# Optimization experiments

Hardware: AMD Instinct MI355X
Metric: run time of the kernel (lower is better)

## Reference

```python
import jax, jax.numpy as jnp
import numpy as np

B, S, T = 128, 1024, 512
VOCAB, E, HE, HD, ATT = 1000, 128, 64, 66, 32


def setup_inputs() -> dict:
    key = jax.random.key(0)
    ks = jax.random.split(key, 14)
    p = lambda k, shape: (jax.random.normal(k, shape, dtype=jnp.float32) * 0.05)
    return {
        'x': jax.random.randint(ks[0], (B, S), 0, VOCAB, dtype=jnp.int32),
        'c': jax.random.normal(ks[1], (B, T), dtype=jnp.float32),
        'emb': p(ks[2], (VOCAB, E)),
        'enc_Wih': p(ks[3], (4 * HE, E)),
        'enc_Whh': p(ks[4], (4 * HE, HE)),
        'enc_b': p(ks[5], (4 * HE,)),
        'att_fc_W': p(ks[6], (HE, E)),
        'att_fc_b': p(ks[7], (HE,)),
        'att_w_W': p(ks[8], (ATT, HE)),
        'att_w_b': p(ks[9], (ATT,)),
        'dec_Wih': p(ks[10], (4 * HD, ATT)),
        'dec_Whh': p(ks[11], (4 * HD, HD)),
        'dec_b': p(ks[12], (4 * HD,)),
        'fin_W': p(ks[13], (E, HD)),
        'fin_b': jnp.zeros((E,), dtype=jnp.float32),
    }


def _lstm_seq(xs, W_ih, W_hh, b, H):
    # xs: [B, S, in]; PyTorch gate order i, f, g, o
    bsz = xs.shape[0]
    gx = jnp.einsum('bsi,gi->bsg', xs, W_ih) + b  # [B,S,4H]

    def step(carry, g_t):
        h, c = carry
        g = g_t + h @ W_hh.T
        i, f, gg, o = jnp.split(g, 4, axis=-1)
        c = jax.nn.sigmoid(f) * c + jax.nn.sigmoid(i) * jnp.tanh(gg)
        h = jax.nn.sigmoid(o) * jnp.tanh(c)
        return (h, c), h

    h0 = jnp.zeros((bsz, H), xs.dtype)
    (_, _), hs = jax.lax.scan(step, (h0, h0), jnp.swapaxes(gx, 0, 1))
    return jnp.swapaxes(hs, 0, 1)  # [B,S,H]


def reference(x, c, emb, enc_Wih, enc_Whh, enc_b, att_fc_W, att_fc_b,
              att_w_W, att_w_b, dec_Wih, dec_Whh, dec_b, fin_W, fin_b):
    # encoder: embed + LSTM, returns full sequence of hidden states [B,S,64]
    enc = _lstm_seq(emb[x], enc_Wih, enc_Whh, enc_b, HE)
    bsz, steps = x.shape[0], c.shape[1]
    # initial decoder input: embedding of token 0, broadcast over batch
    x0 = jnp.broadcast_to(emb[0], (bsz, E))
    h0 = jnp.zeros((bsz, HD), enc.dtype)

    def step(carry, _):
        xemb, h, cc = carry
        # attend(a=xemb, A=enc)
        a = xemb @ att_fc_W.T + att_fc_b                     # [B,64]
        A = a[:, None, :] * enc                              # [B,S,64]
        alpha = jax.nn.softmax(
            jnp.tanh(jnp.einsum('bse,ae->bsa', A, att_w_W) + att_w_b),
            axis=-1)                                         # [B,S,32]
        beta = alpha.sum(axis=1)                             # [B,32]
        # decoder LSTM cell (one timestep)
        g = beta @ dec_Wih.T + h @ dec_Whh.T + dec_b
        i, f, gg, o = jnp.split(g, 4, axis=-1)
        cc = jax.nn.sigmoid(f) * cc + jax.nn.sigmoid(i) * jnp.tanh(gg)
        h = jax.nn.sigmoid(o) * jnp.tanh(cc)
        xemb = h @ fin_W.T + fin_b                           # feed back via final_fc
        return (xemb, h, cc), h

    _, hs = jax.lax.scan(step, (x0, h0, h0), None, length=steps)
    return jnp.swapaxes(hs, 0, 1)  # [B,T,66]
```

## Files before the change

### kernel.cpp

```cpp
#include <hip/hip_runtime.h>
#include <hip/hip_bf16.h>

#define kB 128
#define kS 1024
#define kT 512
#define kV 1000
#define kE 128
#define kHE 64
#define kHD 66
#define kATT 32
#define kGE 256
#define kGD 264

typedef __attribute__((ext_vector_type(4))) float f32x4;
typedef __attribute__((ext_vector_type(8))) short bf16x8;
typedef __attribute__((ext_vector_type(8))) unsigned short u16x8;

__device__ __forceinline__ unsigned short f2bf(float f) {
  unsigned int u = __builtin_bit_cast(unsigned int, f);
  u += 0x7FFFu + ((u >> 16) & 1u);
  return (unsigned short)(u >> 16);
}
__device__ __forceinline__ float rcp_(float x) { return __builtin_amdgcn_rcpf(x); }
__device__ __forceinline__ float fsig(float x)  { return rcp_(1.0f + __expf(-x)); }
__device__ __forceinline__ float ftanh(float x) { return 1.0f - 2.0f * rcp_(1.0f + __expf(2.0f * x)); }
__device__ __forceinline__ float fexp2(float z) {
#if __has_builtin(__builtin_amdgcn_exp2f)
  return __builtin_amdgcn_exp2f(z);
#else
  return __expf(z * 0.6931471805599453f);
#endif
}
__device__ __forceinline__ const unsigned short* launder_us(const unsigned short* p) {
  asm volatile("" : "+s"(p));
  return p;
}
__device__ __forceinline__ float dpp_red16(float v) {
  int x = __builtin_bit_cast(int, v);
  v += __builtin_bit_cast(float, __builtin_amdgcn_update_dpp(0, x, 0xB1, 0xf, 0xf, true));
  x = __builtin_bit_cast(int, v);
  v += __builtin_bit_cast(float, __builtin_amdgcn_update_dpp(0, x, 0x4E, 0xf, 0xf, true));
  x = __builtin_bit_cast(int, v);
  v += __builtin_bit_cast(float, __builtin_amdgcn_update_dpp(0, x, 0x124, 0xf, 0xf, true));
  x = __builtin_bit_cast(int, v);
  v += __builtin_bit_cast(float, __builtin_amdgcn_update_dpp(0, x, 0x128, 0xf, 0xf, true));
  return v;
}
#define DPPB(v, ctrl) __builtin_bit_cast(float, __builtin_amdgcn_update_dpp(0, __builtin_bit_cast(int, (v)), (ctrl), 0xf, 0xf, true))

__global__ __launch_bounds__(256) void prep_kernel(
    const float* __restrict__ emb, const float* __restrict__ enc_Wih,
    const float* __restrict__ enc_b, const float* __restrict__ enc_Whh,
    const float* __restrict__ att_fc_W, const float* __restrict__ att_fc_b,
    const float* __restrict__ att_w_W,
    const float* __restrict__ fin_W, const float* __restrict__ fin_b,
    const float* __restrict__ dec_Wih, const float* __restrict__ dec_Whh,
    const float* __restrict__ dec_b,
    float* __restrict__ embW, unsigned short* __restrict__ decF,
    unsigned short* __restrict__ encF, unsigned short* __restrict__ afF,
    float* __restrict__ wregF, float* __restrict__ dbias,
    float* __restrict__ wh64, float* __restrict__ wh65,
    float* __restrict__ abias, float* __restrict__ ainit) {
  int bid = blockIdx.x, tid = threadIdx.x;
  if (bid < kV) {
    float acc = enc_b[tid];
    const float* er = emb + bid * kE;
    const float* wr = enc_Wih + tid * kE;
    for (int e = 0; e < kE; ++e) acc += er[e] * wr[e];
    embW[bid * kGE + tid] = acc;
  } else if (bid == kV) {
    for (int i = tid; i < 17 * 3 * 64 * 8; i += 256) {
      int jj = i & 7, lane = (i >> 3) & 63, ts = i >> 9;
      int tile = ts / 3, ks = ts - tile * 3;
      int jp = tile * 16 + (lane & 15);
      int cell = jp >> 2, gate = jp & 3;
      int k = ks * 32 + ((lane >> 4) << 3) + jj;
      float v = 0.f;
      if (cell < kHD) {
        int j = gate * kHD + cell;
        if (k < 32) v = dec_Wih[j * kATT + k];
        else v = dec_Whh[j * kHD + (k - 32)];
      }
      decF[i] = f2bf(v);
    }
  } else if (bid == kV + 1) {
    for (int i = tid; i < 16 * 2 * 64 * 8; i += 256) {
      int jj = i & 7, lane = (i >> 3) & 63, ts = i >> 9;
      int tile = ts >> 1, ks = ts & 1;
      int j = tile * 16 + (lane & 15);
      int k = ks * 32 + ((lane >> 4) << 3) + jj;
      encF[i] = f2bf(enc_Whh[j * kHE + k]);
    }
  } else if (bid == kV + 2) {
    for (int i = tid; i < 4 * 3 * 64 * 8; i += 256) {
      int jj = i & 7, lane = (i >> 3) & 63, ts = i >> 9;
      int tile = ts / 3, ks = ts - tile * 3;
      int aidx = tile * 16 + (lane & 15);
      int m = ks * 32 + ((lane >> 4) << 3) + jj;
      float v = 0.f;
      if (m < kHD)
        for (int e = 0; e < kE; ++e) v += att_fc_W[aidx * kE + e] * fin_W[e * kHD + m];
      afF[i] = f2bf(v);
    }
  } else if (bid == kV + 3) {
    for (int i = tid; i < 8 * 64 * 4; i += 256) {
      int c = i & 3, lane = (i >> 2) & 63, jq = i >> 8;
      int half = jq & 1, kc = (jq >> 1) & 1, mt = jq >> 2;
      wregF[i] = att_w_W[(mt * 16 + (lane & 15)) * kHE + kc * 32 + ((lane >> 4) << 3) + half * 4 + c];
    }
  } else if (bid == kV + 4) {
    for (int jp = tid; jp < kGD; jp += 256) {
      int cell = jp >> 2, gate = jp & 3;
      int j = gate * kHD + cell;
      float s = 0.f;
      for (int m = 0; m < kATT; ++m) s += dec_Wih[j * kATT + m];
      dbias[jp] = dec_b[j] + 32.0f * s;
      wh64[jp] = dec_Whh[j * kHD + 64];
      wh65[jp] = dec_Whh[j * kHD + 65];
    }
  } else {
    if (tid < kHE) {
      float acc = att_fc_b[tid];
      for (int e = 0; e < kE; ++e) acc += att_fc_W[tid * kE + e] * fin_b[e];
      abias[tid] = acc;
    } else if (tid < 2 * kHE) {
      int a = tid - kHE;
      float acc = att_fc_b[a];
      for (int e = 0; e < kE; ++e) acc += emb[e] * att_fc_W[a * kE + e];
      ainit[a] = acc;
    }
  }
}

__global__ __launch_bounds__(256)
__attribute__((amdgpu_waves_per_eu(1, 1)))
void enc_kernel(
    const int* __restrict__ x, const float* __restrict__ embW,
    const unsigned short* __restrict__ encF, float* __restrict__ out) {
  __shared__ struct __align__(16) {
    unsigned short xe[64];
    float gbuf[kGE];
    int toks[kS];
  } sm;
  const int b = blockIdx.x, t = threadIdx.x, lane = t & 63, wv = t >> 6;

  for (int i = t; i < kS; i += 256) sm.toks[i] = x[b * kS + i];
  if (t < 64) sm.xe[t] = 0;

  u16x8 eQ[4][2];
  #pragma unroll
  for (int q = 0; q < 4; ++q)
    #pragma unroll
    for (int ks = 0; ks < 2; ++ks)
      eQ[q][ks] = *(const u16x8*)&encF[(((wv * 4 + q) * 2 + ks) * 64 + lane) * 8];
  __syncthreads();

  float gx0 = 0, gx1 = 0, gx2 = 0, gx3 = 0;
  if (lane < 16) {
    int tok = sm.toks[0];
    gx0 = embW[tok * kGE + wv * 64 + 0 + lane];
    gx1 = embW[tok * kGE + wv * 64 + 16 + lane];
    gx2 = embW[tok * kGE + wv * 64 + 32 + lane];
    gx3 = embW[tok * kGE + wv * 64 + 48 + lane];
  }
  float cE = 0.0f;
  unsigned short* eg = (unsigned short*)(out + (size_t)b * (kT * kHD));

  for (int s = 0; s < kS; ++s) {
    union { u16x8 u; bf16x8 v; } xa0, xa1;
    xa0.u = *(const u16x8*)&sm.xe[(lane >> 4) << 3];
    xa1.u = *(const u16x8*)&sm.xe[32 + ((lane >> 4) << 3)];
    float gn0 = 0, gn1 = 0, gn2 = 0, gn3 = 0;
    int tokn = sm.toks[(s + 1 < kS) ? (s + 1) : s];
    if (lane < 16) {
      gn0 = embW[tokn * kGE + wv * 64 + 0 + lane];
      gn1 = embW[tokn * kGE + wv * 64 + 16 + lane];
      gn2 = embW[tokn * kGE + wv * 64 + 32 + lane];
      gn3 = embW[tokn * kGE + wv * 64 + 48 + lane];
    }
    f32x4 z = {0.f, 0.f, 0.f, 0.f};
    f32x4 a0 = __builtin_amdgcn_mfma_f32_16x16x32_bf16(xa0.v, eQ[0][0], z, 0, 0, 0);
    a0 = __builtin_amdgcn_mfma_f32_16x16x32_bf16(xa1.v, eQ[0][1], a0, 0, 0, 0);
    f32x4 a1 = __builtin_amdgcn_mfma_f32_16x16x32_bf16(xa0.v, eQ[1][0], z, 0, 0, 0);
    a1 = __builtin_amdgcn_mfma_f32_16x16x32_bf16(xa1.v, eQ[1][1], a1, 0, 0, 0);
    f32x4 a2 = __builtin_amdgcn_mfma_f32_16x16x32_bf16(xa0.v, eQ[2][0], z, 0, 0, 0);
    a2 = __builtin_amdgcn_mfma_f32_16x16x32_bf16(xa1.v, eQ[2][1], a2, 0, 0, 0);
    f32x4 a3 = __builtin_amdgcn_mfma_f32_16x16x32_bf16(xa0.v, eQ[3][0], z, 0, 0, 0);
    a3 = __builtin_amdgcn_mfma_f32_16x16x32_bf16(xa1.v, eQ[3][1], a3, 0, 0, 0);
    if (lane < 16) {
      sm.gbuf[wv * 64 + 0 + lane]  = a0[0] + gx0;
      sm.gbuf[wv * 64 + 16 + lane] = a1[0] + gx1;
      sm.gbuf[wv * 64 + 32 + lane] = a2[0] + gx2;
      sm.gbuf[wv * 64 + 48 + lane] = a3[0] + gx3;
    }
    __syncthreads();
    if (t < 64) {
      float gi = sm.gbuf[t], gf = sm.gbuf[64 + t], gg = sm.gbuf[128 + t], go = sm.gbuf[192 + t];
      cE = fsig(gf) * cE + fsig(gi) * ftanh(gg);
      float h = fsig(go) * ftanh(cE);
      unsigned short hb = f2bf(h);
      sm.xe[t] = hb;
      eg[s * 64 + ((((t >> 3) ^ (s & 7)) << 3) | (t & 7))] = hb;
    }
    __syncthreads();
    gx0 = gn0; gx1 = gn1; gx2 = gn2; gx3 = gn3;
  }
}

struct __align__(16) DSm {
  unsigned short enc[kS * kHE];
  float wregL[8 * 64 * 4];
  unsigned short afL[4 * 3 * 64 * 8];
  float dbL[kGD];
  float wh64L[kGD];
  float wh65L[kGD];
  float absL[64];
  float aa[64];
  float beta[32];
  unsigned short xv[2][160];
  float hh2[2][2];
};

union U8 { u16x8 u; bf16x8 v; };

__global__ __launch_bounds__(512, 2)
void dec_kernel(
    const float* __restrict__ att_w_b,
    const unsigned short* __restrict__ decF, const unsigned short* __restrict__ afF,
    const float* __restrict__ wregF_ws, const float* __restrict__ dbias_ws,
    const float* __restrict__ wh64_ws, const float* __restrict__ wh65_ws,
    const float* __restrict__ abias_ws, const float* __restrict__ ainit_ws,
    float* __restrict__ out) {
  __shared__ DSm sm;
  const int b = blockIdx.x, t = threadIdx.x, lane = t & 63, wv = t >> 6;
  const int lr = lane & 15, g = lane >> 4;

  {
    const u16x8* src = (const u16x8*)(out + (size_t)b * (kT * kHD));
    u16x8* dst = (u16x8*)sm.enc;
    #pragma unroll
    for (int i = 0; i < 16; ++i) dst[t + i * 512] = src[t + i * 512];
  }
  ((f32x4*)sm.wregL)[t] = ((const f32x4*)wregF_ws)[t];
  for (int i = t; i < 768; i += 512) ((u16x8*)sm.afL)[i] = ((const u16x8*)afF)[i];
  for (int i = t; i < kGD; i += 512) {
    sm.dbL[i] = dbias_ws[i];
    sm.wh64L[i] = wh64_ws[i];
    sm.wh65L[i] = wh65_ws[i];
  }
  if (t < 64) { sm.absL[t] = abias_ws[t]; sm.aa[t] = ainit_ws[t]; }
  if (t < 32) sm.beta[t] = 0.f;
  for (int i = t; i < 320; i += 512) ((unsigned short*)sm.xv)[i] = 0;
  if (t < 4) ((float*)sm.hh2)[t] = 0.f;

  f32x4 wb0, wb1;
  #pragma unroll
  for (int r = 0; r < 4; ++r) {
    wb0[r] = att_w_b[g * 4 + r];
    wb1[r] = att_w_b[16 + g * 4 + r];
  }
  float cDa = 0.0f, cDb = 0.0f, cDc = 0.0f;
  __syncthreads();

  const int sbase = wv * 128;
  const int tileA = wv, tileB = wv + 8;
  const bool has3 = (wv == 7);

  for (int step = 0; step < kT; ++step) {
    const int cb = step & 1, nb = cb ^ 1;
    U8 qa[3], qb[3], qc[3];
    {
      const f32x4* aap = (const f32x4*)sm.aa;
      const f32x4* wrl = (const f32x4*)sm.wregL;
      bf16x8 af[2][2];
      #pragma unroll
      for (int kc = 0; kc < 2; ++kc) {
        f32x4 a0v = aap[kc * 8 + g * 2];
        f32x4 a1v = aap[kc * 8 + g * 2 + 1];
        #pragma unroll
        for (int mt = 0; mt < 2; ++mt) {
          f32x4 w0 = wrl[((mt * 2 + kc) * 2 + 0) * 64 + lane];
          f32x4 w1 = wrl[((mt * 2 + kc) * 2 + 1) * 64 + lane];
          union { bf16x8 v; __hip_bfloat162 h2[4]; } tmp;
          tmp.h2[0] = __float22bfloat162_rn(make_float2(w0.x * a0v.x, w0.y * a0v.y));
          tmp.h2[1] = __float22bfloat162_rn(make_float2(w0.z * a0v.z, w0.w * a0v.w));
          tmp.h2[2] = __float22bfloat162_rn(make_float2(w1.x * a1v.x, w1.y * a1v.y));
          tmp.h2[3] = __float22bfloat162_rn(make_float2(w1.z * a1v.z, w1.w * a1v.w));
          af[mt][kc] = tmp.v;
        }
      }
      float betaAcc[2][4] = {};
      float amax = 0.0f;
      #pragma unroll
      for (int nt = 0; nt < 8; ++nt) {
        int s = sbase + nt * 16 + lr;
        int sw = s & 7;
        U8 e0, e1;
        e0.u = *(const u16x8*)&sm.enc[s * kHE + ((g ^ sw) << 3)];
        e1.u = *(const u16x8*)&sm.enc[s * kHE + (((4 + g) ^ sw) << 3)];
        f32x4 acc0 = __builtin_amdgcn_mfma_f32_16x16x32_bf16(af[0][0], e0.v, wb0, 0, 0, 0);
        acc0 = __builtin_amdgcn_mfma_f32_16x16x32_bf16(af[0][1], e1.v, acc0, 0, 0, 0);
        f32x4 acc1 = __builtin_amdgcn_mfma_f32_16x16x32_bf16(af[1][0], e0.v, wb1, 0, 0, 0);
        acc1 = __builtin_amdgcn_mfma_f32_16x16x32_bf16(af[1][1], e1.v, acc1, 0, 0, 0);
        float u0[4], u1[4], dsum = 0.f;
        #pragma unroll
        for (int r = 0; r < 4; ++r) {
          float x0 = acc0[r], x1 = acc1[r];
          amax = fmaxf(amax, fmaxf(__builtin_fabsf(x0), __builtin_fabsf(x1)));
          u0[r] = fexp2(x0 * __builtin_fmaf(x0 * x0, -0.48089835f, 1.44269504f));
          u1[r] = fexp2(x1 * __builtin_fmaf(x1 * x1, -0.48089835f, 1.44269504f));
          dsum += u0[r] + u1[r];
        }
        dsum += __shfl_xor(dsum, 16);
        dsum += __shfl_xor(dsum, 32);
        float invd = rcp_(dsum);
        #pragma unroll
        for (int r = 0; r < 4; ++r) {
          betaAcc[0][r] += u0[r] * invd;
          betaAcc[1][r] += u1[r] * invd;
        }
      }
      if (__builtin_expect(__any(amax > 0.35f), 0)) {
        #pragma unroll
        for (int mt = 0; mt < 2; ++mt)
          #pragma unroll
          for (int r = 0; r < 4; ++r) betaAcc[mt][r] = 0.f;
        for (int nt = 0; nt < 8; ++nt) {
          int s = sbase + nt * 16 + lr;
          int sw = s & 7;
          U8 e0, e1;
          e0.u = *(const u16x8*)&sm.enc[s * kHE + ((g ^ sw) << 3)];
          e1.u = *(const u16x8*)&sm.enc[s * kHE + (((4 + g) ^ sw) << 3)];
          f32x4 acc0 = __builtin_amdgcn_mfma_f32_16x16x32_bf16(af[0][0], e0.v, wb0, 0, 0, 0);
          acc0 = __builtin_amdgcn_mfma_f32_16x16x32_bf16(af[0][1], e1.v, acc0, 0, 0, 0);
          f32x4 acc1 = __builtin_amdgcn_mfma_f32_16x16x32_bf16(af[1][0], e0.v, wb1, 0, 0, 0);
          acc1 = __builtin_amdgcn_mfma_f32_16x16x32_bf16(af[1][1], e1.v, acc1, 0, 0, 0);
          float u0[4], u1[4], dsum = 0.f;
          for (int r = 0; r < 4; ++r) {
            u0[r] = __expf(tanhf(acc0[r]));
            u1[r] = __expf(tanhf(acc1[r]));
            dsum += u0[r] + u1[r];
          }
          dsum += __shfl_xor(dsum, 16);
          dsum += __shfl_xor(dsum, 32);
          float invd = rcp_(dsum);
          for (int r = 0; r < 4; ++r) {
            betaAcc[0][r] += u0[r] * invd;
            betaAcc[1][r] += u1[r] * invd;
          }
        }
      }
      {
        const unsigned short* dFp = launder_us(decF);
        #pragma unroll
        for (int ks = 0; ks < 3; ++ks) {
          qa[ks].u = *(const u16x8*)&dFp[((tileA * 3 + ks) * 64 + lane) * 8];
          qb[ks].u = *(const u16x8*)&dFp[((tileB * 3 + ks) * 64 + lane) * 8];
        }
        if (has3) {
          #pragma unroll
          for (int ks = 0; ks < 3; ++ks)
            qc[ks].u = *(const u16x8*)&dFp[((16 * 3 + ks) * 64 + lane) * 8];
        }
      }
      #pragma unroll
      for (int mt = 0; mt < 2; ++mt)
        #pragma unroll
        for (int r = 0; r < 4; ++r) {
          float v = dpp_red16(betaAcc[mt][r]);
          if (lr == 0) atomicAdd(&sm.beta[mt * 16 + g * 4 + r], v);
        }
    }
    __syncthreads();
    {
      const f32x4* pb = (const f32x4*)sm.beta;
      f32x4 b0 = pb[g * 2], b1 = pb[g * 2 + 1];
      union { bf16x8 v; __hip_bfloat162 h2[4]; } bfr;
      bfr.h2[0] = __float22bfloat162_rn(make_float2(b0.x - 32.f, b0.y - 32.f));
      bfr.h2[1] = __float22bfloat162_rn(make_float2(b0.z - 32.f, b0.w - 32.f));
      bfr.h2[2] = __float22bfloat162_rn(make_float2(b1.x - 32.f, b1.y - 32.f));
      bfr.h2[3] = __float22bfloat162_rn(make_float2(b1.z - 32.f, b1.w - 32.f));
      U8 xg1, xg2;
      xg1.u = *(const u16x8*)&sm.xv[cb][32 + (g << 3)];
      xg2.u = *(const u16x8*)&sm.xv[cb][64 + (g << 3)];
      float hh0 = sm.hh2[cb][0], hh1 = sm.hh2[cb][1];
      float* op = out + ((size_t)b * kT + step) * kHD;
      const int gate = lane & 3;
      const float kk = (gate == 2) ? 2.0f : 1.0f;
      f32x4 z = {0.f, 0.f, 0.f, 0.f};
      {
        f32x4 ga = __builtin_amdgcn_mfma_f32_16x16x32_bf16(bfr.v, qa[0].v, z, 0, 0, 0);
        ga = __builtin_amdgcn_mfma_f32_16x16x32_bf16(xg1.v, qa[1].v, ga, 0, 0, 0);
        ga = __builtin_amdgcn_mfma_f32_16x16x32_bf16(xg2.v, qa[2].v, ga, 0, 0, 0);
        int jp = tileA * 16 + lr;
        float xg = ga[0] + sm.dbL[jp] + sm.wh64L[jp] * hh0 + sm.wh65L[jp] * hh1;
        float y = fsig(kk * xg);
        float v = (gate == 2) ? (2.0f * y - 1.0f) : y;
        float q0 = DPPB(v, 0x00), q1 = DPPB(v, 0x55), q2 = DPPB(v, 0xAA), q3 = DPPB(v, 0xFF);
        float cn = q1 * cDa + q0 * q2;
        cDa = cn;
        float h = q3 * ftanh(cn);
        if (gate == 0 && lane < 16) {
          int cell = jp >> 2;
          sm.xv[nb][32 + cell] = f2bf(h);
          op[cell] = h;
        }
      }
      {
        f32x4 gb = __builtin_amdgcn_mfma_f32_16x16x32_bf16(bfr.v, qb[0].v, z, 0, 0, 0);
        gb = __builtin_amdgcn_mfma_f32_16x16x32_bf16(xg1.v, qb[1].v, gb, 0, 0, 0);
        gb = __builtin_amdgcn_mfma_f32_16x16x32_bf16(xg2.v, qb[2].v, gb, 0, 0, 0);
        int jp = tileB * 16 + lr;
        float xg = gb[0] + sm.dbL[jp] + sm.wh64L[jp] * hh0 + sm.wh65L[jp] * hh1;
        float y = fsig(kk * xg);
        float v = (gate == 2) ? (2.0f * y - 1.0f) : y;
        float q0 = DPPB(v, 0x00), q1 = DPPB(v, 0x55), q2 = DPPB(v, 0xAA), q3 = DPPB(v, 0xFF);
        float cn = q1 * cDb + q0 * q2;
        cDb = cn;
        float h = q3 * ftanh(cn);
        if (gate == 0 && lane < 16) {
          int cell = jp >> 2;
          sm.xv[nb][32 + cell] = f2bf(h);
          op[cell] = h;
        }
      }
      if (has3) {
        f32x4 gc = __builtin_amdgcn_mfma_f32_16x16x32_bf16(bfr.v, qc[0].v, z, 0, 0, 0);
        gc = __builtin_amdgcn_mfma_f32_16x16x32_bf16(xg1.v, qc[1].v, gc, 0, 0, 0);
        gc = __builtin_amdgcn_mfma_f32_16x16x32_bf16(xg2.v, qc[2].v, gc, 0, 0, 0);
        int jp = 256 + (lane & 7);
        float xg = gc[0] + sm.dbL[jp] + sm.wh64L[jp] * hh0 + sm.wh65L[jp] * hh1;
        float y = fsig(kk * xg);
        float v = (gate == 2) ? (2.0f * y - 1.0f) : y;
        float q0 = DPPB(v, 0x00), q1 = DPPB(v, 0x55), q2 = DPPB(v, 0xAA), q3 = DPPB(v, 0xFF);
        float cn = q1 * cDc + q0 * q2;
        cDc = cn;
        float h = q3 * ftanh(cn);
        if (gate == 0 && lane < 8) {
          int cell = 64 + (lane >> 2);
          sm.xv[nb][32 + cell] = f2bf(h);
          sm.hh2[nb][lane >> 2] = h;
          op[cell] = h;
        }
      }
    }
    __syncthreads();
    if (wv == 0) {
      U8 y0, y1, y2;
      y0.u = *(const u16x8*)&sm.xv[nb][32 + (g << 3)];
      y1.u = *(const u16x8*)&sm.xv[nb][64 + (g << 3)];
      y2.u = *(const u16x8*)&sm.xv[nb][96 + (g << 3)];
      f32x4 z = {0.f, 0.f, 0.f, 0.f};
      #pragma unroll
      for (int tt = 0; tt < 4; ++tt) {
        U8 f0, f1, f2;
        f0.u = *(const u16x8*)&sm.afL[((tt * 3 + 0) * 64 + lane) * 8];
        f1.u = *(const u16x8*)&sm.afL[((tt * 3 + 1) * 64 + lane) * 8];
        f2.u = *(const u16x8*)&sm.afL[((tt * 3 + 2) * 64 + lane) * 8];
        f32x4 acc = __builtin_amdgcn_mfma_f32_16x16x32_bf16(y0.v, f0.v, z, 0, 0, 0);
        acc = __builtin_amdgcn_mfma_f32_16x16x32_bf16(y1.v, f1.v, acc, 0, 0, 0);
        acc = __builtin_amdgcn_mfma_f32_16x16x32_bf16(y2.v, f2.v, acc, 0, 0, 0);
        if (lane < 16) sm.aa[tt * 16 + lane] = acc[0] + sm.absL[tt * 16 + lane];
      }
      if (lane < 32) sm.beta[lane] = 0.f;
    }
    __syncthreads();
  }
}

extern "C" void kernel_launch(void* const* d_in, const int* in_sizes, int n_in,
                              void* d_out, int out_size, void* d_ws, size_t ws_size,
                              hipStream_t stream) {
  const int*   x        = (const int*)d_in[0];
  const float* emb      = (const float*)d_in[2];
  const float* enc_Wih  = (const float*)d_in[3];
  const float* enc_Whh  = (const float*)d_in[4];
  const float* enc_b    = (const float*)d_in[5];
  const float* att_fc_W = (const float*)d_in[6];
  const float* att_fc_b = (const float*)d_in[7];
  const float* att_w_W  = (const float*)d_in[8];
  const float* att_w_b  = (const float*)d_in[9];
  const float* dec_Wih  = (const float*)d_in[10];
  const float* dec_Whh  = (const float*)d_in[11];
  const float* dec_b    = (const float*)d_in[12];
  const float* fin_W    = (const float*)d_in[13];
  const float* fin_b    = (const float*)d_in[14];
  float* out = (float*)d_out;

  float* embW = (float*)d_ws;
  unsigned short* decF = (unsigned short*)(embW + kV * kGE);
  unsigned short* encF = decF + 17 * 3 * 64 * 8;
  unsigned short* afF  = encF + 16 * 2 * 64 * 8;
  float* wregF = (float*)(afF + 4 * 3 * 64 * 8);
  float* dbias = wregF + 8 * 64 * 4;
  float* wh64  = dbias + kGD;
  float* wh65  = wh64 + kGD;
  float* abias = wh65 + kGD;
  float* ainit = abias + kHE;

  prep_kernel<<<dim3(kV + 6), dim3(256), 0, stream>>>(
      emb, enc_Wih, enc_b, enc_Whh, att_fc_W, att_fc_b, att_w_W, fin_W, fin_b,
      dec_Wih, dec_Whh, dec_b, embW, decF, encF, afF, wregF, dbias, wh64, wh65,
      abias, ainit);
  enc_kernel<<<dim3(kB), dim3(256), 0, stream>>>(x, embW, encF, out);
  dec_kernel<<<dim3(kB), dim3(512), 0, stream>>>(
      att_w_b, decF, afF, wregF, dbias, wh64, wh65, abias, ainit, out);
}
```

Measured before the change: 2.823 ms.

## Transpose attention MFMA, split final_fc across four waves with register weights

Swaps the MFMA operands in the attention scoring so each lane holds one attention channel across sequence rows. The softmax denominator then becomes a 16-lane DPP reduction per row, and beta accumulates as two scalars per lane, reduced with two shuffles before the atomics. The final_fc/att_fc projection that fed the next step was done serially by wave 0 over four tiles. It is now split across waves 0-3, each keeping its weight fragment in registers instead of LDS, and wave 4 clears beta. This shortens the serial tail of each decoder step at the cost of more rcp/DPP work per tile and extra registers.

```diff
diff --git a/kernel.cpp b/kernel.cpp
--- a/kernel.cpp
+++ b/kernel.cpp
@@ -210,7 +210,6 @@
 struct __align__(16) DSm {
   unsigned short enc[kS * kHE];
   float wregL[8 * 64 * 4];
-  unsigned short afL[4 * 3 * 64 * 8];
   float dbL[kGD];
   float wh64L[kGD];
   float wh65L[kGD];
@@ -242,7 +241,6 @@
     for (int i = 0; i < 16; ++i) dst[t + i * 512] = src[t + i * 512];
   }
   ((f32x4*)sm.wregL)[t] = ((const f32x4*)wregF_ws)[t];
-  for (int i = t; i < 768; i += 512) ((u16x8*)sm.afL)[i] = ((const u16x8*)afF)[i];
   for (int i = t; i < kGD; i += 512) {
     sm.dbL[i] = dbias_ws[i];
     sm.wh64L[i] = wh64_ws[i];
@@ -253,11 +251,13 @@
   for (int i = t; i < 320; i += 512) ((unsigned short*)sm.xv)[i] = 0;
   if (t < 4) ((float*)sm.hh2)[t] = 0.f;
 
-  f32x4 wb0, wb1;
-  #pragma unroll
-  for (int r = 0; r < 4; ++r) {
-    wb0[r] = att_w_b[g * 4 + r];
-    wb1[r] = att_w_b[16 + g * 4 + r];
+  const float bw0 = att_w_b[lr];
+  const float bw1 = att_w_b[16 + lr];
+  U8 aQ[3];
+  if (wv < 4) {
+    #pragma unroll
+    for (int ks = 0; ks < 3; ++ks)
+      aQ[ks].u = *(const u16x8*)&afF[((wv * 3 + ks) * 64 + lane) * 8];
   }
   float cDa = 0.0f, cDb = 0.0f, cDc = 0.0f;
   __syncthreads();
@@ -289,7 +289,9 @@
           af[mt][kc] = tmp.v;
         }
       }
-      float betaAcc[2][4] = {};
+      f32x4 wc0 = {bw0, bw0, bw0, bw0};
+      f32x4 wc1 = {bw1, bw1, bw1, bw1};
+      float betaAcc[2] = {0.f, 0.f};
       float amax = 0.0f;
       #pragma unroll
       for (int nt = 0; nt < 8; ++nt) {
@@ -298,55 +300,46 @@
         U8 e0, e1;
         e0.u = *(const u16x8*)&sm.enc[s * kHE + ((g ^ sw) << 3)];
         e1.u = *(const u16x8*)&sm.enc[s * kHE + (((4 + g) ^ sw) << 3)];
-        f32x4 acc0 = __builtin_amdgcn_mfma_f32_16x16x32_bf16(af[0][0], e0.v, wb0, 0, 0, 0);
-        acc0 = __builtin_amdgcn_mfma_f32_16x16x32_bf16(af[0][1], e1.v, acc0, 0, 0, 0);
-        f32x4 acc1 = __builtin_amdgcn_mfma_f32_16x16x32_bf16(af[1][0], e0.v, wb1, 0, 0, 0);
-        acc1 = __builtin_amdgcn_mfma_f32_16x16x32_bf16(af[1][1], e1.v, acc1, 0, 0, 0);
-        float u0[4], u1[4], dsum = 0.f;
+        f32x4 acc0 = __builtin_amdgcn_mfma_f32_16x16x32_bf16(e0.v, af[0][0], wc0, 0, 0, 0);
+        acc0 = __builtin_amdgcn_mfma_f32_16x16x32_bf16(e1.v, af[0][1], acc0, 0, 0, 0);
+        f32x4 acc1 = __builtin_amdgcn_mfma_f32_16x16x32_bf16(e0.v, af[1][0], wc1, 0, 0, 0);
+        acc1 = __builtin_amdgcn_mfma_f32_16x16x32_bf16(e1.v, af[1][1], acc1, 0, 0, 0);
+        float u0[4], u1[4];
         #pragma unroll
         for (int r = 0; r < 4; ++r) {
           float x0 = acc0[r], x1 = acc1[r];
           amax = fmaxf(amax, fmaxf(__builtin_fabsf(x0), __builtin_fabsf(x1)));
           u0[r] = fexp2(x0 * __builtin_fmaf(x0 * x0, -0.48089835f, 1.44269504f));
           u1[r] = fexp2(x1 * __builtin_fmaf(x1 * x1, -0.48089835f, 1.44269504f));
-          dsum += u0[r] + u1[r];
-        }
-        dsum += __shfl_xor(dsum, 16);
-        dsum += __shfl_xor(dsum, 32);
-        float invd = rcp_(dsum);
+        }
         #pragma unroll
         for (int r = 0; r < 4; ++r) {
-          betaAcc[0][r] += u0[r] * invd;
-          betaAcc[1][r] += u1[r] * invd;
+          float invd = rcp_(dpp_red16(u0[r] + u1[r]));
+          betaAcc[0] += u0[r] * invd;
+          betaAcc[1] += u1[r] * invd;
         }
       }
       if (__builtin_expect(__any(amax > 0.35f), 0)) {
-        #pragma unroll
-        for (int mt = 0; mt < 2; ++mt)
-          #pragma unroll
-          for (int r = 0; r < 4; ++r) betaAcc[mt][r] = 0.f;
+        betaAcc[0] = 0.f; betaAcc[1] = 0.f;
         for (int nt = 0; nt < 8; ++nt) {
           int s = sbase + nt * 16 + lr;
           int sw = s & 7;
           U8 e0, e1;
           e0.u = *(const u16x8*)&sm.enc[s * kHE + ((g ^ sw) << 3)];
           e1.u = *(const u16x8*)&sm.enc[s * kHE + (((4 + g) ^ sw) << 3)];
-          f32x4 acc0 = __builtin_amdgcn_mfma_f32_16x16x32_bf16(af[0][0], e0.v, wb0, 0, 0, 0);
-          acc0 = __builtin_amdgcn_mfma_f32_16x16x32_bf16(af[0][1], e1.v, acc0, 0, 0, 0);
-          f32x4 acc1 = __builtin_amdgcn_mfma_f32_16x16x32_bf16(af[1][0], e0.v, wb1, 0, 0, 0);
-          acc1 = __builtin_amdgcn_mfma_f32_16x16x32_bf16(af[1][1], e1.v, acc1, 0, 0, 0);
-          float u0[4], u1[4], dsum = 0.f;
+          f32x4 acc0 = __builtin_amdgcn_mfma_f32_16x16x32_bf16(e0.v, af[0][0], wc0, 0, 0, 0);
+          acc0 = __builtin_amdgcn_mfma_f32_16x16x32_bf16(e1.v, af[0][1], acc0, 0, 0, 0);
+          f32x4 acc1 = __builtin_amdgcn_mfma_f32_16x16x32_bf16(e0.v, af[1][0], wc1, 0, 0, 0);
+          acc1 = __builtin_amdgcn_mfma_f32_16x16x32_bf16(e1.v, af[1][1], acc1, 0, 0, 0);
+          float u0[4], u1[4];
           for (int r = 0; r < 4; ++r) {
             u0[r] = __expf(tanhf(acc0[r]));
             u1[r] = __expf(tanhf(acc1[r]));
-            dsum += u0[r] + u1[r];
           }
-          dsum += __shfl_xor(dsum, 16);
-          dsum += __shfl_xor(dsum, 32);
-          float invd = rcp_(dsum);
           for (int r = 0; r < 4; ++r) {
-            betaAcc[0][r] += u0[r] * invd;
-            betaAcc[1][r] += u1[r] * invd;
+            float invd = rcp_(dpp_red16(u0[r] + u1[r]));
+            betaAcc[0] += u0[r] * invd;
+            betaAcc[1] += u1[r] * invd;
           }
         }
       }
@@ -364,12 +357,12 @@
         }
       }
       #pragma unroll
-      for (int mt = 0; mt < 2; ++mt)
-        #pragma unroll
-        for (int r = 0; r < 4; ++r) {
-          float v = dpp_red16(betaAcc[mt][r]);
-          if (lr == 0) atomicAdd(&sm.beta[mt * 16 + g * 4 + r], v);
-        }
+      for (int mt = 0; mt < 2; ++mt) {
+        float v = betaAcc[mt];
+        v += __shfl_xor(v, 16);
+        v += __shfl_xor(v, 32);
+        if (lane < 16) atomicAdd(&sm.beta[mt * 16 + lane], v);
+      }
     }
     __syncthreads();
     {
@@ -445,23 +438,17 @@
       }
     }
     __syncthreads();
-    if (wv == 0) {
+    if (wv < 4) {
       U8 y0, y1, y2;
       y0.u = *(const u16x8*)&sm.xv[nb][32 + (g << 3)];
       y1.u = *(const u16x8*)&sm.xv[nb][64 + (g << 3)];
       y2.u = *(const u16x8*)&sm.xv[nb][96 + (g << 3)];
       f32x4 z = {0.f, 0.f, 0.f, 0.f};
-      #pragma unroll
-      for (int tt = 0; tt < 4; ++tt) {
-        U8 f0, f1, f2;
-        f0.u = *(const u16x8*)&sm.afL[((tt * 3 + 0) * 64 + lane) * 8];
-        f1.u = *(const u16x8*)&sm.afL[((tt * 3 + 1) * 64 + lane) * 8];
-        f2.u = *(const u16x8*)&sm.afL[((tt * 3 + 2) * 64 + lane) * 8];
-        f32x4 acc = __builtin_amdgcn_mfma_f32_16x16x32_bf16(y0.v, f0.v, z, 0, 0, 0);
-        acc = __builtin_amdgcn_mfma_f32_16x16x32_bf16(y1.v, f1.v, acc, 0, 0, 0);
-        acc = __builtin_amdgcn_mfma_f32_16x16x32_bf16(y2.v, f2.v, acc, 0, 0, 0);
-        if (lane < 16) sm.aa[tt * 16 + lane] = acc[0] + sm.absL[tt * 16 + lane];
-      }
+      f32x4 acc = __builtin_amdgcn_mfma_f32_16x16x32_bf16(y0.v, aQ[0].v, z, 0, 0, 0);
+      acc = __builtin_amdgcn_mfma_f32_16x16x32_bf16(y1.v, aQ[1].v, acc, 0, 0, 0);
+      acc = __builtin_amdgcn_mfma_f32_16x16x32_bf16(y2.v, aQ[2].v, acc, 0, 0, 0);
+      if (lane < 16) sm.aa[wv * 16 + lane] = acc[0] + sm.absL[wv * 16 + lane];
+    } else if (wv == 4) {
       if (lane < 32) sm.beta[lane] = 0.f;
     }
     __syncthreads();
```

Result: slower. 2.886 ms (+2.2%).
